# Kernel optimization log

Hardware: AMD Instinct MI355X
Metric: run time of the kernel (lower is better)

## Reference

```python
import jax, jax.numpy as jnp
import numpy as np

N, C, M, P, FL = 2, 512, 8, 1, 4
SPATIAL = [(100, 100), (50, 50), (25, 25), (13, 13)]
S = sum(h * w for h, w in SPATIAL)
CM = C // M


def grid_sample_zeros(im, grid):
    """torch.nn.functional.grid_sample, bilinear, padding_mode='zeros', align_corners=False.
    im: (B, Cc, H, W); grid: (B, Hg, Wg, 2) with grid[...,0]=x, grid[...,1]=y in [-1,1].
    Returns (B, Cc, Hg, Wg)."""
    B, Cc, H, W = im.shape
    Hg, Wg = grid.shape[1], grid.shape[2]
    x = (grid[..., 0] + 1.0) * (W * 0.5) - 0.5
    y = (grid[..., 1] + 1.0) * (H * 0.5) - 0.5
    x0f = jnp.floor(x)
    y0f = jnp.floor(y)
    wx1 = x - x0f
    wy1 = y - y0f
    wx0 = 1.0 - wx1
    wy0 = 1.0 - wy1
    x0 = x0f.astype(jnp.int32)
    y0 = y0f.astype(jnp.int32)
    flat = im.reshape(B, Cc, H * W)

    def gather(ix, iy):
        valid = ((ix >= 0) & (ix < W) & (iy >= 0) & (iy < H)).astype(im.dtype)
        idx = jnp.clip(iy, 0, H - 1) * W + jnp.clip(ix, 0, W - 1)  # (B,Hg,Wg)
        idx = jnp.broadcast_to(idx.reshape(B, 1, Hg * Wg), (B, Cc, Hg * Wg))
        v = jnp.take_along_axis(flat, idx, axis=2).reshape(B, Cc, Hg, Wg)
        return v * valid[:, None]

    out = (gather(x0, y0) * (wx0 * wy0)[:, None]
           + gather(x0 + 1, y0) * (wx1 * wy0)[:, None]
           + gather(x0, y0 + 1) * (wx0 * wy1)[:, None]
           + gather(x0 + 1, y0 + 1) * (wx1 * wy1)[:, None])
    return out


def setup_inputs() -> dict:
    key = jax.random.key(0)
    ks = jax.random.split(key, 8)
    x = jax.random.normal(ks[0], (N, C, S), jnp.float32)
    pos = jax.random.normal(ks[1], (N, C, S), jnp.float32)
    key_padding_mask = jnp.zeros((N, S), jnp.bool_)
    # valid (W,H) per level; no padding -> full size, scale 1
    valid_sizes = jnp.broadcast_to(
        jnp.array([[w, h] for (h, w) in SPATIAL], jnp.float32)[None], (N, FL, 2))
    valid_scales = jnp.ones((N, FL, 2), jnp.float32)
    s = 1.0 / np.sqrt(C)
    Wv = (jax.random.normal(ks[2], (C, C), jnp.float32) * s)
    bv = jnp.zeros((C,), jnp.float32)
    Wloc = jax.random.normal(ks[3], (M * FL * P * 2, C), jnp.float32) * 0.01
    # torch bias init: head-direction grid, channel layout (M, F, P, 2)
    grid_init = np.array([-1, -1, -1, 0, -1, 1, 0, -1, 0, 1, 1, -1, 1, 0, 1, 1],
                         np.float32).reshape(M, 1, 1, 2)
    grid_init = np.tile(grid_init, (1, FL, P, 1))
    for i in range(P):
        grid_init[:, :, i, :] *= (i + 1)
    bloc = jnp.asarray(grid_init.reshape(-1))
    Ww = jax.random.normal(ks[4], (M * FL * P, C), jnp.float32) * 0.01
    bw = jnp.zeros((M * FL * P,), jnp.float32)
    Wo = (jax.random.normal(ks[5], (C, C), jnp.float32) * s)
    bo = jnp.zeros((C,), jnp.float32)
    scale = jnp.ones((C,), jnp.float32)
    return dict(x=x, pos=pos, key_padding_mask=key_padding_mask,
                valid_sizes=valid_sizes, valid_scales=valid_scales,
                Wv=Wv, bv=bv, Wloc=Wloc, bloc=bloc, Ww=Ww, bw=bw,
                Wo=Wo, bo=bo, scale=scale)


def reference(x, pos, key_padding_mask, valid_sizes, valid_scales,
              Wv, bv, Wloc, bloc, Ww, bw, Wo, bo, scale):
    mask = key_padding_mask[:, None, :]  # (N,1,S)
    x_pos = jnp.where(mask, 0.0, x + pos)
    value = jnp.einsum('oc,ncs->nos', Wv, x) + bv[:, None]
    value = jnp.where(mask, 0.0, value)

    # per-level value maps, split heads: (N*M, C/M, H, W)
    values, cur = [], 0
    for (H, W) in SPATIAL:
        values.append(value[..., cur:cur + H * W].reshape(N * M, CM, H, W))
        cur += H * W

    vs = jnp.repeat(valid_sizes, M, axis=0)          # (NM, F, 2) = repeat_interleave
    vc2 = jnp.repeat(2.0 * valid_scales, M, axis=0)  # (NM, F, 2)

    outs, cur = [], 0
    for lvl, (H, W) in enumerate(SPATIAL):
        L = H * W
        xp = x_pos[..., cur:cur + L]  # (N, C, L)
        cur += L
        # 1x1 convs == per-token linears
        off = jnp.einsum('oc,ncl->nol', Wloc, xp) + bloc[:, None]
        off = off.reshape(N * M, FL, P, 2, L).transpose(0, 1, 2, 4, 3)  # (NM,F,P,L,2)
        w = jnp.einsum('oc,ncl->nol', Ww, xp) + bw[:, None]
        w = jax.nn.softmax(w.reshape(N * M, 1, FL * P, L), axis=2)
        # pixel-center grid of the query level, (L,2) as (x,y)
        ys, xs = jnp.meshgrid(jnp.arange(H, dtype=jnp.float32) + 0.5,
                              jnp.arange(W, dtype=jnp.float32) + 0.5, indexing='ij')
        pre = jnp.stack([xs, ys], -1).reshape(L, 2)
        sc = (vc2 / vs[:, lvl:lvl + 1])[:, :, None, None, :]  # (NM,F,1,1,2)
        grids = off * sc + (pre[None, None, None] * sc - 1.0)  # (NM,F,P,L,2)
        samples = jnp.concatenate(
            [grid_sample_zeros(values[f], grids[:, f]) for f in range(FL)], axis=2)  # (NM,CM,F*P,L)
        out = jnp.sum(samples * w, axis=2).reshape(N, C, L)
        out = jnp.einsum('oc,ncl->nol', Wo, out) + bo[:, None]
        outs.append(out)
    return jnp.concatenate(outs, axis=-1) * scale[None, :, None]
```

## Files before the change

kernel.cpp:

```cpp
#include <hip/hip_runtime.h>
#include <math.h>

#define TOT_S   13294
#define NBATCH  2
#define CCH     512
#define MHEAD   8
#define PITCH   40

typedef short     short8  __attribute__((ext_vector_type(8)));
typedef float     f32x4   __attribute__((ext_vector_type(4)));
typedef unsigned short u16x8 __attribute__((ext_vector_type(8)));
typedef unsigned short u16x4 __attribute__((ext_vector_type(4)));

__device__ __forceinline__ unsigned short f2bf(float f) {
    union { float f; unsigned int u; } v; v.f = f;
    unsigned int r = v.u + 0x7fffu + ((v.u >> 16) & 1u);
    return (unsigned short)(r >> 16);
}
__device__ __forceinline__ float bf2f(unsigned short h) {
    union { unsigned int u; float f; } v; v.u = ((unsigned int)h) << 16;
    return v.f;
}

__global__ void cast_f32_bf16(const float* __restrict__ src,
                              unsigned short* __restrict__ dst, int n4)
{
    const int i = blockIdx.x * blockDim.x + threadIdx.x;
    if (i < n4) {
        const float4 v = *(const float4*)(src + (size_t)i * 4);
        u16x4 o;
        o[0] = f2bf(v.x); o[1] = f2bf(v.y); o[2] = f2bf(v.z); o[3] = f2bf(v.w);
        *(u16x4*)(dst + (size_t)i * 4) = o;
    }
}

__global__ __launch_bounds__(256)
void cast_transpose(const float* __restrict__ x, const float* __restrict__ pos,
                    const unsigned char* __restrict__ mask,
                    unsigned short* __restrict__ xbt,
                    unsigned short* __restrict__ xpbt)
{
    const int lane = threadIdx.x;
    const int n = blockIdx.z;
    const int s = blockIdx.x * 64 + lane;
    if (s >= TOT_S) return;
    const int cb = (blockIdx.y * 4 + threadIdx.y) * 8;
    const float* xp = x   + ((size_t)n * CCH + cb) * TOT_S + s;
    const float* pp = pos + ((size_t)n * CCH + cb) * TOT_S + s;
    const bool mk = mask[(size_t)n * TOT_S + s] != 0;
    u16x8 vx, vp;
#pragma unroll
    for (int j = 0; j < 8; ++j) {
        const float a = xp[(size_t)j * TOT_S];
        const float b = pp[(size_t)j * TOT_S];
        vx[j] = f2bf(a);
        vp[j] = mk ? (unsigned short)0 : f2bf(a + b);
    }
    const size_t o = ((size_t)n * TOT_S + s) * CCH + cb;
    *(u16x8*)(xbt + o)  = vx;
    *(u16x8*)(xpbt + o) = vp;
}

__global__ __launch_bounds__(256)
void gemm_value_mfma(const unsigned short* __restrict__ Wb,
                     const unsigned short* __restrict__ Act,
                     const float* __restrict__ bv,
                     const unsigned char* __restrict__ mask,
                     unsigned short* __restrict__ valb)
{
    __shared__ unsigned short Wl[128 * PITCH];
    __shared__ unsigned short Al[128 * PITCH];
    const int n  = blockIdx.z;
    const int ob = blockIdx.y * 128;
    const int sb = blockIdx.x * 128;
    const int tid = threadIdx.x;
    const int r   = tid >> 1;
    const int seg = (tid & 1) * 16;
    const unsigned short* wsrc = Wb + ((size_t)(ob + r)) * CCH + seg;
    const int sr = min(sb + r, TOT_S - 1);
    const unsigned short* asrc = Act + ((size_t)n * TOT_S + sr) * CCH + seg;
    unsigned short* wdst = &Wl[r * PITCH + seg];
    unsigned short* adst = &Al[r * PITCH + seg];

    const int wave = tid >> 6, lane = tid & 63;
    const int m0 = (wave & 1) * 64, n0 = (wave >> 1) * 64;
    const int row16 = lane & 15, q = lane >> 4;

    u16x8 w0 = *(const u16x8*)(wsrc);
    u16x8 w1 = *(const u16x8*)(wsrc + 8);
    u16x8 a0 = *(const u16x8*)(asrc);
    u16x8 a1 = *(const u16x8*)(asrc + 8);

    f32x4 acc[4][4] = {};
    for (int k0 = 0; k0 < CCH; k0 += 32) {
        *(u16x8*)wdst = w0; *(u16x8*)(wdst + 8) = w1;
        *(u16x8*)adst = a0; *(u16x8*)(adst + 8) = a1;
        __syncthreads();
        if (k0 + 32 < CCH) {
            w0 = *(const u16x8*)(wsrc + k0 + 32);
            w1 = *(const u16x8*)(wsrc + k0 + 40);
            a0 = *(const u16x8*)(asrc + k0 + 32);
            a1 = *(const u16x8*)(asrc + k0 + 40);
        }
        short8 af[4], bfr[4];
#pragma unroll
        for (int mt = 0; mt < 4; ++mt)
            af[mt] = *(const short8*)&Wl[(m0 + mt * 16 + row16) * PITCH + q * 8];
#pragma unroll
        for (int nt = 0; nt < 4; ++nt)
            bfr[nt] = *(const short8*)&Al[(n0 + nt * 16 + row16) * PITCH + q * 8];
#pragma unroll
        for (int mt = 0; mt < 4; ++mt)
#pragma unroll
            for (int nt = 0; nt < 4; ++nt)
                acc[mt][nt] = __builtin_amdgcn_mfma_f32_16x16x32_bf16(
                    af[mt], bfr[nt], acc[mt][nt], 0, 0, 0);
        __syncthreads();
    }

#pragma unroll
    for (int nt = 0; nt < 4; ++nt) {
        const int s = sb + n0 + nt * 16 + row16;
        if (s >= TOT_S) continue;
        const float msk = mask[(size_t)n * TOT_S + s] ? 0.f : 1.f;
        unsigned short* orow = valb + ((size_t)n * TOT_S + s) * CCH + ob + m0;
#pragma unroll
        for (int mt = 0; mt < 4; ++mt) {
            const f32x4 bvv = *(const f32x4*)(bv + ob + m0 + mt * 16 + q * 4);
            const f32x4 a = acc[mt][nt];
            u16x4 ov;
            ov[0] = f2bf((a[0] + bvv[0]) * msk);
            ov[1] = f2bf((a[1] + bvv[1]) * msk);
            ov[2] = f2bf((a[2] + bvv[2]) * msk);
            ov[3] = f2bf((a[3] + bvv[3]) * msk);
            *(u16x4*)(orow + mt * 16 + q * 4) = ov;
        }
    }
}

__global__ __launch_bounds__(256)
void gemm_offw_mfma(const unsigned short* __restrict__ Wlb,
                    const unsigned short* __restrict__ Wwb,
                    const float* __restrict__ bloc, const float* __restrict__ bw,
                    const unsigned short* __restrict__ Act,
                    float* __restrict__ offw)
{
    __shared__ unsigned short Wl[128 * PITCH];
    __shared__ unsigned short Al[128 * PITCH];
    const int n  = blockIdx.z;
    const int sb = blockIdx.x * 128;
    const int tid = threadIdx.x;
    const int r   = tid >> 1;
    const int seg = (tid & 1) * 16;
    const bool wzero = (r >= 96);
    const unsigned short* wsrc =
        (r < 64) ? (Wlb + (size_t)r * CCH + seg)
                 : (Wwb + (size_t)((r < 96 ? r : 95) - 64) * CCH + seg);
    const int sr = min(sb + r, TOT_S - 1);
    const unsigned short* asrc = Act + ((size_t)n * TOT_S + sr) * CCH + seg;
    unsigned short* wdst = &Wl[r * PITCH + seg];
    unsigned short* adst = &Al[r * PITCH + seg];

    const int wave = tid >> 6, lane = tid & 63;
    const int m0 = (wave & 1) * 64, n0 = (wave >> 1) * 64;
    const int row16 = lane & 15, q = lane >> 4;

    u16x8 w0 = {}, w1 = {};
    if (!wzero) { w0 = *(const u16x8*)(wsrc); w1 = *(const u16x8*)(wsrc + 8); }
    u16x8 a0 = *(const u16x8*)(asrc);
    u16x8 a1 = *(const u16x8*)(asrc + 8);

    f32x4 acc[4][4] = {};
    for (int k0 = 0; k0 < CCH; k0 += 32) {
        *(u16x8*)wdst = w0; *(u16x8*)(wdst + 8) = w1;
        *(u16x8*)adst = a0; *(u16x8*)(adst + 8) = a1;
        __syncthreads();
        if (k0 + 32 < CCH) {
            if (!wzero) {
                w0 = *(const u16x8*)(wsrc + k0 + 32);
                w1 = *(const u16x8*)(wsrc + k0 + 40);
            }
            a0 = *(const u16x8*)(asrc + k0 + 32);
            a1 = *(const u16x8*)(asrc + k0 + 40);
        }
        short8 af[4], bfr[4];
#pragma unroll
        for (int mt = 0; mt < 4; ++mt)
            af[mt] = *(const short8*)&Wl[(m0 + mt * 16 + row16) * PITCH + q * 8];
#pragma unroll
        for (int nt = 0; nt < 4; ++nt)
            bfr[nt] = *(const short8*)&Al[(n0 + nt * 16 + row16) * PITCH + q * 8];
#pragma unroll
        for (int mt = 0; mt < 4; ++mt)
#pragma unroll
            for (int nt = 0; nt < 4; ++nt)
                acc[mt][nt] = __builtin_amdgcn_mfma_f32_16x16x32_bf16(
                    af[mt], bfr[nt], acc[mt][nt], 0, 0, 0);
        __syncthreads();
    }

#pragma unroll
    for (int nt = 0; nt < 4; ++nt) {
        const int s = sb + n0 + nt * 16 + row16;
        if (s >= TOT_S) continue;
        float* orow = offw + ((size_t)n * TOT_S + s) * 96;
#pragma unroll
        for (int mt = 0; mt < 4; ++mt) {
            const int o = m0 + mt * 16 + q * 4;
            if (o < 96) {
                const float* bsrc = (o < 64) ? (bloc + o) : (bw + o - 64);
                const f32x4 bb = *(const f32x4*)bsrc;
                f32x4 v = acc[mt][nt];
                v[0] += bb[0]; v[1] += bb[1]; v[2] += bb[2]; v[3] += bb[3];
                *(f32x4*)(orow + o) = v;
            }
        }
    }
}

__global__ __launch_bounds__(256)
void sample_attn(const unsigned short* __restrict__ value,
                 const float* __restrict__ offw,
                 const float* __restrict__ vsizes,
                 const float* __restrict__ vscales,
                 unsigned short* __restrict__ samp)
{
    const int lane = threadIdx.x;
    const int item = blockIdx.x * blockDim.y + threadIdx.y;
    const int total = NBATCH * TOT_S;
    if (item >= total) return;
    const int s = item % TOT_S;
    const int n = item / TOT_S;
    const int m = lane >> 3;

    int lvl; float prex, prey;
    if (s < 10000)      { lvl = 0; const int l = s;         const int qq = l / 100; prey = qq + 0.5f; prex = (l - qq * 100) + 0.5f; }
    else if (s < 12500) { lvl = 1; const int l = s - 10000; const int qq = l / 50;  prey = qq + 0.5f; prex = (l - qq * 50)  + 0.5f; }
    else if (s < 13125) { lvl = 2; const int l = s - 12500; const int qq = l / 25;  prey = qq + 0.5f; prex = (l - qq * 25)  + 0.5f; }
    else                { lvl = 3; const int l = s - 13125; const int qq = l / 13;  prey = qq + 0.5f; prex = (l - qq * 13)  + 0.5f; }

    const float* ow = offw + ((size_t)n * TOT_S + s) * 96;

    const float w0 = ow[64 + m * 4 + 0], w1 = ow[64 + m * 4 + 1];
    const float w2 = ow[64 + m * 4 + 2], w3 = ow[64 + m * 4 + 3];
    const float mx = fmaxf(fmaxf(w0, w1), fmaxf(w2, w3));
    const float e0 = expf(w0 - mx), e1 = expf(w1 - mx), e2 = expf(w2 - mx), e3 = expf(w3 - mx);
    const float inv = 1.f / (e0 + e1 + e2 + e3);
    const float wgt[4] = { e0 * inv, e1 * inv, e2 * inv, e3 * inv };

    const int HS[4]  = { 100, 50, 25, 13 };
    const int WS[4]  = { 100, 50, 25, 13 };
    const int CUR[4] = { 0, 10000, 12500, 13125 };

    const float invsx = 1.f / vsizes[((n * 4) + lvl) * 2 + 0];
    const float invsy = 1.f / vsizes[((n * 4) + lvl) * 2 + 1];
    const unsigned short* vbase = value + (size_t)n * TOT_S * CCH + lane * 8;

    float acc[8] = {};
#pragma unroll
    for (int f = 0; f < 4; ++f) {
        const float offx = ow[(m * 4 + f) * 2 + 0];
        const float offy = ow[(m * 4 + f) * 2 + 1];
        const float scx = 2.f * vscales[((n * 4) + f) * 2 + 0] * invsx;
        const float scy = 2.f * vscales[((n * 4) + f) * 2 + 1] * invsy;
        const int Wf = WS[f], Hf = HS[f], cf = CUR[f];
        const float xi = (offx + prex) * scx * (Wf * 0.5f) - 0.5f;
        const float yi = (offy + prey) * scy * (Hf * 0.5f) - 0.5f;
        const float x0f = floorf(xi), y0f = floorf(yi);
        const float wx1 = xi - x0f, wy1 = yi - y0f;
        const float wx0 = 1.f - wx1, wy0 = 1.f - wy1;
        const int x0 = (int)x0f, y0 = (int)y0f;
        const bool xin0 = (x0 >= 0) && (x0 < Wf);
        const bool xin1 = (x0 + 1 >= 0) && (x0 + 1 < Wf);
        const bool yin0 = (y0 >= 0) && (y0 < Hf);
        const bool yin1 = (y0 + 1 >= 0) && (y0 + 1 < Hf);
        const float cw00 = (xin0 && yin0) ? wgt[f] * wx0 * wy0 : 0.f;
        const float cw10 = (xin1 && yin0) ? wgt[f] * wx1 * wy0 : 0.f;
        const float cw01 = (xin0 && yin1) ? wgt[f] * wx0 * wy1 : 0.f;
        const float cw11 = (xin1 && yin1) ? wgt[f] * wx1 * wy1 : 0.f;
        const int x0c = min(max(x0, 0), Wf - 1);
        const int x1c = min(max(x0 + 1, 0), Wf - 1);
        const int y0c = min(max(y0, 0), Hf - 1);
        const int y1c = min(max(y0 + 1, 0), Hf - 1);
        const unsigned short* row0 = vbase + (size_t)(cf + y0c * Wf) * CCH;
        const unsigned short* row1 = vbase + (size_t)(cf + y1c * Wf) * CCH;
        const u16x8 v00 = *(const u16x8*)(row0 + (size_t)x0c * CCH);
        const u16x8 v10 = *(const u16x8*)(row0 + (size_t)x1c * CCH);
        const u16x8 v01 = *(const u16x8*)(row1 + (size_t)x0c * CCH);
        const u16x8 v11 = *(const u16x8*)(row1 + (size_t)x1c * CCH);
#pragma unroll
        for (int j = 0; j < 8; ++j) {
            acc[j] += cw00 * bf2f(v00[j]) + cw10 * bf2f(v10[j])
                    + cw01 * bf2f(v01[j]) + cw11 * bf2f(v11[j]);
        }
    }

    u16x8 ov;
#pragma unroll
    for (int j = 0; j < 8; ++j) ov[j] = f2bf(acc[j]);
    *(u16x8*)(samp + ((size_t)n * TOT_S + s) * CCH + lane * 8) = ov;
}

__global__ __launch_bounds__(256)
void gemm_out_mfma(const unsigned short* __restrict__ Wob,
                   const unsigned short* __restrict__ Sampb,
                   const float* __restrict__ bo, const float* __restrict__ scale,
                   float* __restrict__ out)
{
    __shared__ unsigned short Sl[128 * PITCH];
    __shared__ unsigned short Wl[128 * PITCH];
    const int n  = blockIdx.z;
    const int ob = blockIdx.y * 128;
    const int sb = blockIdx.x * 128;
    const int tid = threadIdx.x;
    const int r   = tid >> 1;
    const int seg = (tid & 1) * 16;
    const int sr = min(sb + r, TOT_S - 1);
    const unsigned short* ssrc = Sampb + ((size_t)n * TOT_S + sr) * CCH + seg;
    const unsigned short* wsrc = Wob + ((size_t)(ob + r)) * CCH + seg;
    unsigned short* sdst = &Sl[r * PITCH + seg];
    unsigned short* wdst = &Wl[r * PITCH + seg];

    const int wave = tid >> 6, lane = tid & 63;
    const int m0 = (wave & 1) * 64, n0 = (wave >> 1) * 64;
    const int row16 = lane & 15, q = lane >> 4;

    u16x8 s0v = *(const u16x8*)(ssrc);
    u16x8 s1v = *(const u16x8*)(ssrc + 8);
    u16x8 w0v = *(const u16x8*)(wsrc);
    u16x8 w1v = *(const u16x8*)(wsrc + 8);

    f32x4 acc[4][4] = {};
    for (int k0 = 0; k0 < CCH; k0 += 32) {
        *(u16x8*)sdst = s0v; *(u16x8*)(sdst + 8) = s1v;
        *(u16x8*)wdst = w0v; *(u16x8*)(wdst + 8) = w1v;
        __syncthreads();
        if (k0 + 32 < CCH) {
            s0v = *(const u16x8*)(ssrc + k0 + 32);
            s1v = *(const u16x8*)(ssrc + k0 + 40);
            w0v = *(const u16x8*)(wsrc + k0 + 32);
            w1v = *(const u16x8*)(wsrc + k0 + 40);
        }
        short8 af[4], bfr[4];
#pragma unroll
        for (int mt = 0; mt < 4; ++mt)
            af[mt] = *(const short8*)&Sl[(m0 + mt * 16 + row16) * PITCH + q * 8];
#pragma unroll
        for (int nt = 0; nt < 4; ++nt)
            bfr[nt] = *(const short8*)&Wl[(n0 + nt * 16 + row16) * PITCH + q * 8];
#pragma unroll
        for (int mt = 0; mt < 4; ++mt)
#pragma unroll
            for (int nt = 0; nt < 4; ++nt)
                acc[mt][nt] = __builtin_amdgcn_mfma_f32_16x16x32_bf16(
                    af[mt], bfr[nt], acc[mt][nt], 0, 0, 0);
        __syncthreads();
    }

#pragma unroll
    for (int nt = 0; nt < 4; ++nt) {
        const int o = ob + n0 + nt * 16 + row16;
        const float bo_ = bo[o];
        const float sc_ = scale[o];
        float* orow = out + ((size_t)n * CCH + o) * (size_t)TOT_S;
#pragma unroll
        for (int mt = 0; mt < 4; ++mt) {
            const int s0 = sb + m0 + mt * 16 + q * 4;
            const f32x4 a = acc[mt][nt];
            if (s0 + 3 < TOT_S) {
                float2 v0 = make_float2((a[0] + bo_) * sc_, (a[1] + bo_) * sc_);
                float2 v1 = make_float2((a[2] + bo_) * sc_, (a[3] + bo_) * sc_);
                *(float2*)(orow + s0) = v0;
                *(float2*)(orow + s0 + 2) = v1;
            } else {
                for (int i = 0; i < 4; ++i)
                    if (s0 + i < TOT_S) orow[s0 + i] = (a[i] + bo_) * sc_;
            }
        }
    }
}

extern "C" void kernel_launch(void* const* d_in, const int* in_sizes, int n_in,
                              void* d_out, int out_size, void* d_ws, size_t ws_size,
                              hipStream_t stream)
{
    const float* x     = (const float*)d_in[0];
    const float* pos   = (const float*)d_in[1];
    const unsigned char* mask = (const unsigned char*)d_in[2];
    const float* vsz   = (const float*)d_in[3];
    const float* vsc   = (const float*)d_in[4];
    const float* Wv    = (const float*)d_in[5];
    const float* bv    = (const float*)d_in[6];
    const float* Wloc  = (const float*)d_in[7];
    const float* bloc  = (const float*)d_in[8];
    const float* Ww    = (const float*)d_in[9];
    const float* bw    = (const float*)d_in[10];
    const float* Wo    = (const float*)d_in[11];
    const float* bo    = (const float*)d_in[12];
    const float* scale = (const float*)d_in[13];
    float* out = (float*)d_out;

    const size_t SC = (size_t)TOT_S * CCH;
    unsigned short* valb  = (unsigned short*)d_ws;
    unsigned short* sampb = valb  + 2 * SC;
    unsigned short* xbt   = sampb + 2 * SC;
    unsigned short* xpbt  = xbt   + 2 * SC;
    float* offw = (float*)(xpbt + 2 * SC);
    unsigned short* wvb = (unsigned short*)(offw + 2 * (size_t)TOT_S * 96);
    unsigned short* wob = wvb + 512 * 512;
    unsigned short* wlb = wob + 512 * 512;
    unsigned short* wwb = wlb + 64 * 512;

    cast_f32_bf16<<<256, 256, 0, stream>>>(Wv,   wvb, 512 * 512 / 4);
    cast_f32_bf16<<<256, 256, 0, stream>>>(Wo,   wob, 512 * 512 / 4);
    cast_f32_bf16<<<32,  256, 0, stream>>>(Wloc, wlb, 64 * 512 / 4);
    cast_f32_bf16<<<16,  256, 0, stream>>>(Ww,   wwb, 32 * 512 / 4);

    cast_transpose<<<dim3((TOT_S + 63) / 64, 16, NBATCH), dim3(64, 4), 0, stream>>>(
        x, pos, mask, xbt, xpbt);

    const int sTiles = (TOT_S + 127) / 128;

    gemm_value_mfma<<<dim3(sTiles, CCH / 128, NBATCH), 256, 0, stream>>>(
        wvb, xbt, bv, mask, valb);
    gemm_offw_mfma<<<dim3(sTiles, 1, NBATCH), 256, 0, stream>>>(
        wlb, wwb, bloc, bw, xpbt, offw);

    const int items = NBATCH * TOT_S;
    sample_attn<<<(items + 3) / 4, dim3(64, 4), 0, stream>>>(valb, offw, vsz, vsc, sampb);

    gemm_out_mfma<<<dim3(sTiles, CCH / 128, NBATCH), 256, 0, stream>>>(
        wob, sampb, bo, scale, out);
}
```

Baseline: 316.8 us.

## Fuse fp32-to-bf16 cast-transpose into GEMM activation loaders

Removes the separate cast_transpose kernel and its bf16 transposed activation buffers. The value and offset/weight GEMMs now load fp32 x (and pos, with the mask) directly in channel-major layout, convert to bf16, and transpose into shared memory inside the K loop. This saves one kernel launch and the write and re-read of intermediate buffers. In exchange, each GEMM block reads fp32 activations redundantly across output tiles and does scattered 4-byte LDS stores.

```diff
diff --git a/kernel.cpp b/kernel.cpp
--- a/kernel.cpp
+++ b/kernel.cpp
@@ -35,35 +35,8 @@
 }
 
 __global__ __launch_bounds__(256)
-void cast_transpose(const float* __restrict__ x, const float* __restrict__ pos,
-                    const unsigned char* __restrict__ mask,
-                    unsigned short* __restrict__ xbt,
-                    unsigned short* __restrict__ xpbt)
-{
-    const int lane = threadIdx.x;
-    const int n = blockIdx.z;
-    const int s = blockIdx.x * 64 + lane;
-    if (s >= TOT_S) return;
-    const int cb = (blockIdx.y * 4 + threadIdx.y) * 8;
-    const float* xp = x   + ((size_t)n * CCH + cb) * TOT_S + s;
-    const float* pp = pos + ((size_t)n * CCH + cb) * TOT_S + s;
-    const bool mk = mask[(size_t)n * TOT_S + s] != 0;
-    u16x8 vx, vp;
-#pragma unroll
-    for (int j = 0; j < 8; ++j) {
-        const float a = xp[(size_t)j * TOT_S];
-        const float b = pp[(size_t)j * TOT_S];
-        vx[j] = f2bf(a);
-        vp[j] = mk ? (unsigned short)0 : f2bf(a + b);
-    }
-    const size_t o = ((size_t)n * TOT_S + s) * CCH + cb;
-    *(u16x8*)(xbt + o)  = vx;
-    *(u16x8*)(xpbt + o) = vp;
-}
-
-__global__ __launch_bounds__(256)
 void gemm_value_mfma(const unsigned short* __restrict__ Wb,
-                     const unsigned short* __restrict__ Act,
+                     const float* __restrict__ x,
                      const float* __restrict__ bv,
                      const unsigned char* __restrict__ mask,
                      unsigned short* __restrict__ valb)
@@ -74,13 +47,15 @@
     const int ob = blockIdx.y * 128;
     const int sb = blockIdx.x * 128;
     const int tid = threadIdx.x;
+
     const int r   = tid >> 1;
     const int seg = (tid & 1) * 16;
     const unsigned short* wsrc = Wb + ((size_t)(ob + r)) * CCH + seg;
-    const int sr = min(sb + r, TOT_S - 1);
-    const unsigned short* asrc = Act + ((size_t)n * TOT_S + sr) * CCH + seg;
     unsigned short* wdst = &Wl[r * PITCH + seg];
-    unsigned short* adst = &Al[r * PITCH + seg];
+
+    const int sp   = tid & 15;
+    const int cpid = tid >> 4;
+    const size_t XLIM = (size_t)NBATCH * CCH * TOT_S - 2;
 
     const int wave = tid >> 6, lane = tid & 63;
     const int m0 = (wave & 1) * 64, n0 = (wave >> 1) * 64;
@@ -88,19 +63,44 @@
 
     u16x8 w0 = *(const u16x8*)(wsrc);
     u16x8 w1 = *(const u16x8*)(wsrc + 8);
-    u16x8 a0 = *(const u16x8*)(asrc);
-    u16x8 a1 = *(const u16x8*)(asrc + 8);
+    float2 ax[2][4];
+#pragma unroll
+    for (int cc = 0; cc < 2; ++cc)
+#pragma unroll
+        for (int j = 0; j < 4; ++j) {
+            size_t off = ((size_t)n * CCH + 2 * cpid + cc) * TOT_S
+                       + sb + 2 * sp + 32 * j;
+            off = off > XLIM ? XLIM : off;
+            ax[cc][j] = *(const float2*)(x + off);
+        }
 
     f32x4 acc[4][4] = {};
     for (int k0 = 0; k0 < CCH; k0 += 32) {
         *(u16x8*)wdst = w0; *(u16x8*)(wdst + 8) = w1;
-        *(u16x8*)adst = a0; *(u16x8*)(adst + 8) = a1;
+#pragma unroll
+        for (int j = 0; j < 4; ++j)
+#pragma unroll
+            for (int i = 0; i < 2; ++i) {
+                const int s = 2 * sp + 32 * j + i;
+                const float lo = i ? ax[0][j].y : ax[0][j].x;
+                const float hi = i ? ax[1][j].y : ax[1][j].x;
+                const unsigned int pk =
+                    (unsigned int)f2bf(lo) | ((unsigned int)f2bf(hi) << 16);
+                *(unsigned int*)&Al[(size_t)s * PITCH + 2 * cpid] = pk;
+            }
         __syncthreads();
         if (k0 + 32 < CCH) {
             w0 = *(const u16x8*)(wsrc + k0 + 32);
             w1 = *(const u16x8*)(wsrc + k0 + 40);
-            a0 = *(const u16x8*)(asrc + k0 + 32);
-            a1 = *(const u16x8*)(asrc + k0 + 40);
+#pragma unroll
+            for (int cc = 0; cc < 2; ++cc)
+#pragma unroll
+                for (int j = 0; j < 4; ++j) {
+                    size_t off = ((size_t)n * CCH + k0 + 32 + 2 * cpid + cc) * TOT_S
+                               + sb + 2 * sp + 32 * j;
+                    off = off > XLIM ? XLIM : off;
+                    ax[cc][j] = *(const float2*)(x + off);
+                }
         }
         short8 af[4], bfr[4];
 #pragma unroll
@@ -142,7 +142,8 @@
 void gemm_offw_mfma(const unsigned short* __restrict__ Wlb,
                     const unsigned short* __restrict__ Wwb,
                     const float* __restrict__ bloc, const float* __restrict__ bw,
-                    const unsigned short* __restrict__ Act,
+                    const float* __restrict__ x, const float* __restrict__ pos,
+                    const unsigned char* __restrict__ mask,
                     float* __restrict__ offw)
 {
     __shared__ unsigned short Wl[128 * PITCH];
@@ -150,16 +151,27 @@
     const int n  = blockIdx.z;
     const int sb = blockIdx.x * 128;
     const int tid = threadIdx.x;
+
     const int r   = tid >> 1;
     const int seg = (tid & 1) * 16;
     const bool wzero = (r >= 96);
     const unsigned short* wsrc =
         (r < 64) ? (Wlb + (size_t)r * CCH + seg)
                  : (Wwb + (size_t)((r < 96 ? r : 95) - 64) * CCH + seg);
-    const int sr = min(sb + r, TOT_S - 1);
-    const unsigned short* asrc = Act + ((size_t)n * TOT_S + sr) * CCH + seg;
     unsigned short* wdst = &Wl[r * PITCH + seg];
-    unsigned short* adst = &Al[r * PITCH + seg];
+
+    const int sp   = tid & 15;
+    const int cpid = tid >> 4;
+    const size_t XLIM = (size_t)NBATCH * CCH * TOT_S - 2;
+    float mkm[8];
+#pragma unroll
+    for (int j = 0; j < 4; ++j)
+#pragma unroll
+        for (int i = 0; i < 2; ++i) {
+            const int s = sb + 2 * sp + 32 * j + i;
+            const int sc = s < TOT_S ? s : TOT_S - 1;
+            mkm[j * 2 + i] = mask[(size_t)n * TOT_S + sc] ? 0.f : 1.f;
+        }
 
     const int wave = tid >> 6, lane = tid & 63;
     const int m0 = (wave & 1) * 64, n0 = (wave >> 1) * 64;
@@ -167,21 +179,50 @@
 
     u16x8 w0 = {}, w1 = {};
     if (!wzero) { w0 = *(const u16x8*)(wsrc); w1 = *(const u16x8*)(wsrc + 8); }
-    u16x8 a0 = *(const u16x8*)(asrc);
-    u16x8 a1 = *(const u16x8*)(asrc + 8);
+    float2 ax[2][4], ap[2][4];
+#pragma unroll
+    for (int cc = 0; cc < 2; ++cc)
+#pragma unroll
+        for (int j = 0; j < 4; ++j) {
+            size_t off = ((size_t)n * CCH + 2 * cpid + cc) * TOT_S
+                       + sb + 2 * sp + 32 * j;
+            off = off > XLIM ? XLIM : off;
+            ax[cc][j] = *(const float2*)(x + off);
+            ap[cc][j] = *(const float2*)(pos + off);
+        }
 
     f32x4 acc[4][4] = {};
     for (int k0 = 0; k0 < CCH; k0 += 32) {
         *(u16x8*)wdst = w0; *(u16x8*)(wdst + 8) = w1;
-        *(u16x8*)adst = a0; *(u16x8*)(adst + 8) = a1;
+#pragma unroll
+        for (int j = 0; j < 4; ++j)
+#pragma unroll
+            for (int i = 0; i < 2; ++i) {
+                const int s = 2 * sp + 32 * j + i;
+                const float lo = (i ? ax[0][j].y + ap[0][j].y
+                                    : ax[0][j].x + ap[0][j].x) * mkm[j * 2 + i];
+                const float hi = (i ? ax[1][j].y + ap[1][j].y
+                                    : ax[1][j].x + ap[1][j].x) * mkm[j * 2 + i];
+                const unsigned int pk =
+                    (unsigned int)f2bf(lo) | ((unsigned int)f2bf(hi) << 16);
+                *(unsigned int*)&Al[(size_t)s * PITCH + 2 * cpid] = pk;
+            }
         __syncthreads();
         if (k0 + 32 < CCH) {
             if (!wzero) {
                 w0 = *(const u16x8*)(wsrc + k0 + 32);
                 w1 = *(const u16x8*)(wsrc + k0 + 40);
             }
-            a0 = *(const u16x8*)(asrc + k0 + 32);
-            a1 = *(const u16x8*)(asrc + k0 + 40);
+#pragma unroll
+            for (int cc = 0; cc < 2; ++cc)
+#pragma unroll
+                for (int j = 0; j < 4; ++j) {
+                    size_t off = ((size_t)n * CCH + k0 + 32 + 2 * cpid + cc) * TOT_S
+                               + sb + 2 * sp + 32 * j;
+                    off = off > XLIM ? XLIM : off;
+                    ax[cc][j] = *(const float2*)(x + off);
+                    ap[cc][j] = *(const float2*)(pos + off);
+                }
         }
         short8 af[4], bfr[4];
 #pragma unroll
@@ -403,9 +444,7 @@
     const size_t SC = (size_t)TOT_S * CCH;
     unsigned short* valb  = (unsigned short*)d_ws;
     unsigned short* sampb = valb  + 2 * SC;
-    unsigned short* xbt   = sampb + 2 * SC;
-    unsigned short* xpbt  = xbt   + 2 * SC;
-    float* offw = (float*)(xpbt + 2 * SC);
+    float* offw = (float*)(sampb + 2 * SC);
     unsigned short* wvb = (unsigned short*)(offw + 2 * (size_t)TOT_S * 96);
     unsigned short* wob = wvb + 512 * 512;
     unsigned short* wlb = wob + 512 * 512;
@@ -416,15 +455,12 @@
     cast_f32_bf16<<<32,  256, 0, stream>>>(Wloc, wlb, 64 * 512 / 4);
     cast_f32_bf16<<<16,  256, 0, stream>>>(Ww,   wwb, 32 * 512 / 4);
 
-    cast_transpose<<<dim3((TOT_S + 63) / 64, 16, NBATCH), dim3(64, 4), 0, stream>>>(
-        x, pos, mask, xbt, xpbt);
-
     const int sTiles = (TOT_S + 127) / 128;
 
     gemm_value_mfma<<<dim3(sTiles, CCH / 128, NBATCH), 256, 0, stream>>>(
-        wvb, xbt, bv, mask, valb);
+        wvb, x, bv, mask, valb);
     gemm_offw_mfma<<<dim3(sTiles, 1, NBATCH), 256, 0, stream>>>(
-        wlb, wwb, bloc, bw, xpbt, offw);
+        wlb, wwb, bloc, bw, x, pos, mask, offw);
 
     const int items = NBATCH * TOT_S;
     sample_attn<<<(items + 3) / 4, dim3(64, 4), 0, stream>>>(valb, offw, vsz, vsc, sampb);
```

New measurement: 291.1 us. -8.1%, faster.
